# Kernel optimization log

Measured on AMD Instinct MI355X. Metric: run time of the kernel, lower is better.

The kernel has to match this reference:

```python
import jax, jax.numpy as jnp
import numpy as np

E, CAP, D = 32, 4096, 256
H = 4 * D  # hidden_dim = 4*d_model


def setup_inputs() -> dict:
    key = jax.random.key(0)
    k1, k2, k3 = jax.random.split(key, 3)
    x = jax.random.normal(k1, (E, CAP, D), dtype=jnp.float32)
    w_fc = jax.random.normal(k2, (E, D, H), dtype=jnp.float32) * (1.0 / np.sqrt(D))
    w_proj = jax.random.normal(k3, (E, H, D), dtype=jnp.float32) * (1.0 / np.sqrt(H))
    return {"x": x, "w_fc": w_fc, "w_proj": w_proj}


def reference(x, w_fc, w_proj):
    # h = bmm(x, w_fc): [E, cap, d] @ [E, d, 4d] -> [E, cap, 4d]
    h = jnp.einsum('ecd,edh->ech', x, w_fc)
    # exact GELU (torch nn.GELU default uses erf form)
    h = jax.nn.gelu(h, approximate=False)
    # out = bmm(h, w_proj): [E, cap, 4d] @ [E, 4d, d] -> [E, cap, d]
    out = jnp.einsum('ech,ehd->ecd', h, w_proj)
    # dropout is identity in eval mode (p=0.0 here)
    return out
```

## Files before the change

kernel.cpp:

```cpp
#include <hip/hip_runtime.h>
#include <cstdint>
#include <cstddef>


#define NE   32
#define CAPN 4096
#define DDIM 256
#define HDIM 1024

typedef __bf16 bf16x8 __attribute__((ext_vector_type(8)));
typedef __bf16 bf16x4 __attribute__((ext_vector_type(4)));
typedef __bf16 bf16x2 __attribute__((ext_vector_type(2)));
typedef float  f32x4  __attribute__((ext_vector_type(4)));

#define XS_OFF   0
#define STG_OFF  65536
#define STG_SZ   16384
#define HC_OFF   98304
#define LDS_BYTES 131072

#define AS1 __attribute__((address_space(1)))
#define AS3 __attribute__((address_space(3)))

__device__ __forceinline__ void gld_lds16(const void* g, void* l) {
  __builtin_amdgcn_global_load_lds((const AS1 uint32_t*)g, (AS3 uint32_t*)l, 16, 0, 0);
}

__device__ __forceinline__ float gelu_f(float x) {
  float x2 = x * x;
  float u  = x * __builtin_fmaf(0.1029432f, x2, 2.3022078f);
  float t  = __builtin_amdgcn_exp2f(u);
  float r  = __builtin_amdgcn_rcpf(t + 1.0f);
  return __builtin_fmaf(-x, r, x);
}

__global__ __launch_bounds__(256) void tcast_kernel(const float* __restrict__ in,
                                                    __bf16* __restrict__ outp,
                                                    int R, int C) {
  __shared__ __bf16 tl[64][72];
  const int cb = C >> 6;
  const int nb = (R >> 6) * cb;
  const int b  = blockIdx.x;
  const int e  = b / nb;
  const int t  = b - e * nb;
  const int br = t / cb;
  const int bc = t - br * cb;
  const float* src = in + ((size_t)e * R + (size_t)br * 64) * C + (size_t)bc * 64;
#pragma unroll
  for (int i = 0; i < 16; ++i) {
    int idx = i * 256 + threadIdx.x;
    int r = idx >> 6, c = idx & 63;
    tl[c][r] = (__bf16)src[(size_t)r * C + c];
  }
  __syncthreads();
  __bf16* dst = outp + ((size_t)e * C + (size_t)bc * 64) * R + (size_t)br * 64;
#pragma unroll
  for (int i = 0; i < 8; ++i) {
    int idx = i * 512 + threadIdx.x * 2;
    int c = idx >> 6, r = idx & 63;
    bf16x2 p;
    p[0] = tl[c][r];
    p[1] = tl[c][r + 1];
    *(bf16x2*)(dst + (size_t)c * R + r) = p;
  }
}

__global__ __launch_bounds__(512, 2) void fused_mlp(
    const float* __restrict__ x, const __bf16* __restrict__ wfcT,
    const __bf16* __restrict__ wprojT, float* __restrict__ out) {
  extern __shared__ char smem[];
  const int tid  = threadIdx.x;
  const int lane = tid & 63;
  const int l15  = lane & 15;
  const int l4   = lane >> 4;
  const int w    = tid >> 6;
  const int wm   = w & 1;
  const int q    = w >> 1;
  const int bid  = blockIdx.x;
  const int e    = bid >> 5;
  const int m0   = (bid & 31) << 7;

  auto stage_slab = [&](int s) {
    const int buf = s & 1;
    const int c   = s >> 3;
    const int t   = s & 7;
    const __bf16* base;
    size_t rs;
    if (t < 4) {
      base = wfcT + (size_t)(e * HDIM + c * 128) * DDIM + t * 64;
      rs   = DDIM;
    } else {
      const int j = t - 4;
      base = wprojT + (size_t)(e * DDIM + (j & 1) * 128) * HDIM + c * 128 + (j >> 1) * 64;
      rs   = HDIM;
    }
#pragma unroll
    for (int i = 0; i < 2; ++i) {
      int o  = tid + i * 512;
      int r  = o >> 3;
      int sl = (o & 7) ^ (r & 7);
      gld_lds16(base + (size_t)r * rs + sl * 8, &smem[STG_OFF + buf * STG_SZ + o * 16]);
    }
  };

  {
    const float* xb = x + ((size_t)(e * CAPN + m0)) * DDIM;
#pragma unroll
    for (int i = 0; i < 8; ++i) {
      int f2  = i * 512 + tid;
      int row = f2 >> 5;
      int s   = f2 & 31;
      const float4 a0 = *(const float4*)(xb + (size_t)row * DDIM + s * 8);
      const float4 a1 = *(const float4*)(xb + (size_t)row * DDIM + s * 8 + 4);
      bf16x8 v;
      v[0] = (__bf16)a0.x; v[1] = (__bf16)a0.y; v[2] = (__bf16)a0.z; v[3] = (__bf16)a0.w;
      v[4] = (__bf16)a1.x; v[5] = (__bf16)a1.y; v[6] = (__bf16)a1.z; v[7] = (__bf16)a1.w;
      int phys = (s & 24) | ((s & 7) ^ (row & 7));
      *(bf16x8*)(&smem[XS_OFF + row * 512 + phys * 16]) = v;
    }
  }

  stage_slab(0);
  stage_slab(1);

  f32x4 zero = 0.0f;
  f32x4 acc2[4][4];
#pragma unroll
  for (int a = 0; a < 4; ++a)
#pragma unroll
    for (int b = 0; b < 4; ++b) acc2[a][b] = zero;

#define SLAB_PRE(lastp)                                                        \
  do {                                                                         \
    if (lastp) asm volatile("s_waitcnt vmcnt(0) lgkmcnt(0)" ::: "memory");     \
    else       asm volatile("s_waitcnt vmcnt(2) lgkmcnt(0)" ::: "memory");     \
    __builtin_amdgcn_s_barrier();                                              \
    __builtin_amdgcn_sched_barrier(0);                                         \
  } while (0)

#define SLAB_POST(sidx)                                                        \
  do {                                                                         \
    __builtin_amdgcn_sched_barrier(0);                                         \
    __builtin_amdgcn_s_barrier();                                              \
    if ((sidx) + 2 < 64) stage_slab((sidx) + 2);                               \
  } while (0)

  for (int c = 0; c < 8; ++c) {
    f32x4 acc1[2][4];
#pragma unroll
    for (int a = 0; a < 2; ++a)
#pragma unroll
      for (int b = 0; b < 4; ++b) acc1[a][b] = zero;

#pragma unroll
    for (int ks = 0; ks < 4; ++ks) {
      const int sidx = c * 8 + ks;
      const int buf  = sidx & 1;
      SLAB_PRE(false);
      bf16x8 a0[2], a1[2], b0[4], b1[4];
#pragma unroll
      for (int fh = 0; fh < 2; ++fh) {
        int r = q * 32 + fh * 16 + l15;
        a0[fh] = *(const bf16x8*)(&smem[STG_OFF + buf * STG_SZ + r * 128 + ((0 * 4 + l4) ^ (r & 7)) * 16]);
        a1[fh] = *(const bf16x8*)(&smem[STG_OFF + buf * STG_SZ + r * 128 + ((1 * 4 + l4) ^ (r & 7)) * 16]);
      }
#pragma unroll
      for (int fm = 0; fm < 4; ++fm) {
        int m   = wm * 64 + fm * 16 + l15;
        int sl0 = ks * 8 + 0 * 4 + l4;
        int sl1 = ks * 8 + 1 * 4 + l4;
        int p0  = (sl0 & 24) | ((sl0 & 7) ^ (m & 7));
        int p1  = (sl1 & 24) | ((sl1 & 7) ^ (m & 7));
        b0[fm] = *(const bf16x8*)(&smem[XS_OFF + m * 512 + p0 * 16]);
        b1[fm] = *(const bf16x8*)(&smem[XS_OFF + m * 512 + p1 * 16]);
      }
      __builtin_amdgcn_s_setprio(1);
#pragma unroll
      for (int fh = 0; fh < 2; ++fh)
#pragma unroll
        for (int fm = 0; fm < 4; ++fm)
          acc1[fh][fm] = __builtin_amdgcn_mfma_f32_16x16x32_bf16(a0[fh], b0[fm], acc1[fh][fm], 0, 0, 0);
#pragma unroll
      for (int fh = 0; fh < 2; ++fh)
#pragma unroll
        for (int fm = 0; fm < 4; ++fm)
          acc1[fh][fm] = __builtin_amdgcn_mfma_f32_16x16x32_bf16(a1[fh], b1[fm], acc1[fh][fm], 0, 0, 0);
      __builtin_amdgcn_s_setprio(0);
      SLAB_POST(sidx);
    }

#pragma unroll
    for (int fh = 0; fh < 2; ++fh) {
#pragma unroll
      for (int fm = 0; fm < 4; ++fm) {
        int m  = wm * 64 + fm * 16 + l15;
        int hl = q * 32 + fh * 16 + l4 * 4;
        bf16x4 hv;
#pragma unroll
        for (int j = 0; j < 4; ++j) hv[j] = (__bf16)gelu_f(acc1[fh][fm][j]);
        int sl   = hl >> 3;
        int half = (hl >> 2) & 1;
        int ph   = (sl & 8) | ((sl & 7) ^ (m & 7));
        *(bf16x4*)(&smem[HC_OFF + m * 256 + ph * 16 + half * 8]) = hv;
      }
    }

#pragma unroll
    for (int j = 0; j < 4; ++j) {
      const int sidx = c * 8 + 4 + j;
      const int buf  = sidx & 1;
      const int hd   = j & 1;
      const int hh   = j >> 1;
      const bool last = (c == 7) && (j == 3);
      SLAB_PRE(last);
      bf16x8 a0[2], a1[2], b0[4], b1[4];
#pragma unroll
      for (int fd = 0; fd < 2; ++fd) {
        int r = q * 32 + fd * 16 + l15;
        a0[fd] = *(const bf16x8*)(&smem[STG_OFF + buf * STG_SZ + r * 128 + ((0 * 4 + l4) ^ (r & 7)) * 16]);
        a1[fd] = *(const bf16x8*)(&smem[STG_OFF + buf * STG_SZ + r * 128 + ((1 * 4 + l4) ^ (r & 7)) * 16]);
      }
#pragma unroll
      for (int fm = 0; fm < 4; ++fm) {
        int m   = wm * 64 + fm * 16 + l15;
        int sl0 = hh * 8 + 0 * 4 + l4;
        int sl1 = hh * 8 + 1 * 4 + l4;
        int p0  = (sl0 & 8) | ((sl0 & 7) ^ (m & 7));
        int p1  = (sl1 & 8) | ((sl1 & 7) ^ (m & 7));
        b0[fm] = *(const bf16x8*)(&smem[HC_OFF + m * 256 + p0 * 16]);
        b1[fm] = *(const bf16x8*)(&smem[HC_OFF + m * 256 + p1 * 16]);
      }
      __builtin_amdgcn_s_setprio(1);
#pragma unroll
      for (int fd = 0; fd < 2; ++fd)
#pragma unroll
        for (int fm = 0; fm < 4; ++fm)
          acc2[hd * 2 + fd][fm] = __builtin_amdgcn_mfma_f32_16x16x32_bf16(a0[fd], b0[fm], acc2[hd * 2 + fd][fm], 0, 0, 0);
#pragma unroll
      for (int fd = 0; fd < 2; ++fd)
#pragma unroll
        for (int fm = 0; fm < 4; ++fm)
          acc2[hd * 2 + fd][fm] = __builtin_amdgcn_mfma_f32_16x16x32_bf16(a1[fd], b1[fm], acc2[hd * 2 + fd][fm], 0, 0, 0);
      __builtin_amdgcn_s_setprio(0);
      SLAB_POST(sidx);
    }
  }

#pragma unroll
  for (int a = 0; a < 4; ++a) {
#pragma unroll
    for (int fm = 0; fm < 4; ++fm) {
      int m = m0 + wm * 64 + fm * 16 + l15;
      int d = (a >> 1) * 128 + q * 32 + (a & 1) * 16 + l4 * 4;
      *(f32x4*)(out + ((size_t)(e * CAPN + m)) * DDIM + d) = acc2[a][fm];
    }
  }
}

extern "C" void kernel_launch(void* const* d_in, const int* in_sizes, int n_in,
                              void* d_out, int out_size, void* d_ws, size_t ws_size,
                              hipStream_t stream) {
  (void)in_sizes; (void)n_in; (void)out_size; (void)ws_size;
  const float* x     = (const float*)d_in[0];
  const float* wfc   = (const float*)d_in[1];
  const float* wproj = (const float*)d_in[2];
  float* out = (float*)d_out;

  __bf16* wfcT   = (__bf16*)d_ws;
  __bf16* wprojT = (__bf16*)((char*)d_ws + (size_t)NE * DDIM * HDIM * sizeof(__bf16));

  hipFuncSetAttribute((const void*)fused_mlp,
                      hipFuncAttributeMaxDynamicSharedMemorySize, LDS_BYTES);

  tcast_kernel<<<dim3(NE * 64), dim3(256), 0, stream>>>(wfc, wfcT, DDIM, HDIM);
  tcast_kernel<<<dim3(NE * 64), dim3(256), 0, stream>>>(wproj, wprojT, HDIM, DDIM);
  fused_mlp<<<dim3(NE * 32), dim3(512), LDS_BYTES, stream>>>(x, wfcT, wprojT, out);
}
```

Before: 243.9 us.

## Add 160KB-LDS fused MLP variant with 256-wide hidden chunks

Adds a new fused MLP kernel that uses 160KB of LDS to hold a full 128x256 hidden chunk and processes the hidden dimension in 4 chunks of 256 instead of 8 of 128. It uses a 4x4 MFMA tile per wave with thinner 32-wide k slabs. Larger hidden chunks reduce the number of GELU/phase transitions and let each wave cover more output per slab. The cost is occupancy, which drops from 2 blocks to 1 block per CU, leaving less latency hiding. The old 128KB kernel stays as a fallback if the larger LDS attribute is rejected.

```diff
diff --git a/kernel.cpp b/kernel.cpp
--- a/kernel.cpp
+++ b/kernel.cpp
@@ -12,12 +12,6 @@
 typedef __bf16 bf16x4 __attribute__((ext_vector_type(4)));
 typedef __bf16 bf16x2 __attribute__((ext_vector_type(2)));
 typedef float  f32x4  __attribute__((ext_vector_type(4)));
-
-#define XS_OFF   0
-#define STG_OFF  65536
-#define STG_SZ   16384
-#define HC_OFF   98304
-#define LDS_BYTES 131072
 
 #define AS1 __attribute__((address_space(1)))
 #define AS3 __attribute__((address_space(3)))
@@ -33,6 +27,28 @@
   float r  = __builtin_amdgcn_rcpf(t + 1.0f);
   return __builtin_fmaf(-x, r, x);
 }
+
+#define SLAB_PRE(lastp)                                                        \
+  do {                                                                         \
+    if (lastp) asm volatile("s_waitcnt vmcnt(0) lgkmcnt(0)" ::: "memory");     \
+    else       asm volatile("s_waitcnt vmcnt(2) lgkmcnt(0)" ::: "memory");     \
+    __builtin_amdgcn_s_barrier();                                              \
+    __builtin_amdgcn_sched_barrier(0);                                         \
+  } while (0)
+
+#define SLAB_POST_160(sidx)                                                    \
+  do {                                                                         \
+    __builtin_amdgcn_sched_barrier(0);                                         \
+    __builtin_amdgcn_s_barrier();                                              \
+    if ((sidx) + 2 < 64) stage_slab((sidx) + 2);                               \
+  } while (0)
+
+#define SLAB_POST_128(sidx)                                                    \
+  do {                                                                         \
+    __builtin_amdgcn_sched_barrier(0);                                         \
+    __builtin_amdgcn_s_barrier();                                              \
+    if ((sidx) + 2 < 64) stage_slab((sidx) + 2);                               \
+  } while (0)
 
 __global__ __launch_bounds__(256) void tcast_kernel(const float* __restrict__ in,
                                                     __bf16* __restrict__ outp,
@@ -65,7 +81,13 @@
   }
 }
 
-__global__ __launch_bounds__(512, 2) void fused_mlp(
+#define B_XS   0
+#define B_HC   65536
+#define B_STG  131072
+#define STG_SZ 16384
+#define LDS160 163840
+
+__global__ __launch_bounds__(512, 1) void fused_mlp_160(
     const float* __restrict__ x, const __bf16* __restrict__ wfcT,
     const __bf16* __restrict__ wprojT, float* __restrict__ out) {
   extern __shared__ char smem[];
@@ -80,6 +102,168 @@
   const int e    = bid >> 5;
   const int m0   = (bid & 31) << 7;
 
+  const int physA = l4 ^ ((l15 >> 1) & 3);
+  const int aBase = B_STG + q * 4096 + l15 * 64 + physA * 16;
+  const int mRow  = wm * 64 + l15;
+  const int m7    = l15 & 7;
+
+  auto stage_slab = [&](int s) {
+    const int buf = s & 1;
+    const int c   = s >> 4;
+    const int t   = s & 15;
+    const __bf16* base;
+    size_t rs;
+    if (t < 8) {
+      base = wfcT + (size_t)(e * HDIM + c * 256) * DDIM + t * 32;
+      rs   = DDIM;
+    } else {
+      base = wprojT + (size_t)(e * DDIM) * HDIM + c * 256 + (t - 8) * 32;
+      rs   = HDIM;
+    }
+#pragma unroll
+    for (int i = 0; i < 2; ++i) {
+      int o  = tid + i * 512;
+      int r  = o >> 2;
+      int sl = (o & 3) ^ ((r >> 1) & 3);
+      gld_lds16(base + (size_t)r * rs + sl * 8, &smem[B_STG + buf * STG_SZ + o * 16]);
+    }
+  };
+
+  {
+    const float* xb = x + ((size_t)(e * CAPN + m0)) * DDIM;
+#pragma unroll
+    for (int i = 0; i < 8; ++i) {
+      int f2  = i * 512 + tid;
+      int row = f2 >> 5;
+      int s   = f2 & 31;
+      const float4 a0 = *(const float4*)(xb + (size_t)row * DDIM + s * 8);
+      const float4 a1 = *(const float4*)(xb + (size_t)row * DDIM + s * 8 + 4);
+      bf16x8 v;
+      v[0] = (__bf16)a0.x; v[1] = (__bf16)a0.y; v[2] = (__bf16)a0.z; v[3] = (__bf16)a0.w;
+      v[4] = (__bf16)a1.x; v[5] = (__bf16)a1.y; v[6] = (__bf16)a1.z; v[7] = (__bf16)a1.w;
+      int phys = (s & 24) | ((s & 7) ^ (row & 7));
+      *(bf16x8*)(&smem[B_XS + row * 512 + phys * 16]) = v;
+    }
+  }
+
+  stage_slab(0);
+  stage_slab(1);
+
+  f32x4 zero = 0.0f;
+  f32x4 acc2[4][4];
+#pragma unroll
+  for (int a = 0; a < 4; ++a)
+#pragma unroll
+    for (int b = 0; b < 4; ++b) acc2[a][b] = zero;
+
+  for (int c = 0; c < 4; ++c) {
+    f32x4 acc1[4][4];
+#pragma unroll
+    for (int a = 0; a < 4; ++a)
+#pragma unroll
+      for (int b = 0; b < 4; ++b) acc1[a][b] = zero;
+
+#pragma unroll
+    for (int ds = 0; ds < 8; ++ds) {
+      const int sidx = c * 16 + ds;
+      const int buf  = ds & 1;
+      SLAB_PRE(false);
+      bf16x8 af[4], bx[4];
+#pragma unroll
+      for (int f = 0; f < 4; ++f)
+        af[f] = *(const bf16x8*)(&smem[aBase + buf * STG_SZ + f * 1024]);
+#pragma unroll
+      for (int fm = 0; fm < 4; ++fm) {
+        int s  = ds * 4 + l4;
+        int ph = (s & 24) | ((s & 7) ^ m7);
+        bx[fm] = *(const bf16x8*)(&smem[B_XS + (mRow + fm * 16) * 512 + ph * 16]);
+      }
+      __builtin_amdgcn_s_setprio(1);
+#pragma unroll
+      for (int fa = 0; fa < 4; ++fa)
+#pragma unroll
+        for (int fm = 0; fm < 4; ++fm)
+          acc1[fa][fm] = __builtin_amdgcn_mfma_f32_16x16x32_bf16(
+              af[fa], bx[fm], acc1[fa][fm], 0, 0, 0);
+      __builtin_amdgcn_s_setprio(0);
+      SLAB_POST_160(sidx);
+    }
+
+#pragma unroll
+    for (int fa = 0; fa < 4; ++fa) {
+#pragma unroll
+      for (int fm = 0; fm < 4; ++fm) {
+        int m  = mRow + fm * 16;
+        int s  = q * 8 + fa * 2 + (l4 >> 1);
+        int hf = l4 & 1;
+        bf16x4 hv;
+#pragma unroll
+        for (int j = 0; j < 4; ++j) hv[j] = (__bf16)gelu_f(acc1[fa][fm][j]);
+        int ph = (s & 24) | ((s & 7) ^ (m & 7));
+        *(bf16x4*)(&smem[B_HC + m * 512 + ph * 16 + hf * 8]) = hv;
+      }
+    }
+
+#pragma unroll
+    for (int hs = 0; hs < 8; ++hs) {
+      const int sidx = c * 16 + 8 + hs;
+      const int buf  = hs & 1;
+      const bool last = (hs == 7) && (c == 3);
+      SLAB_PRE(last);
+      bf16x8 af[4], bx[4];
+#pragma unroll
+      for (int f = 0; f < 4; ++f)
+        af[f] = *(const bf16x8*)(&smem[aBase + buf * STG_SZ + f * 1024]);
+#pragma unroll
+      for (int fm = 0; fm < 4; ++fm) {
+        int s  = hs * 4 + l4;
+        int ph = (s & 24) | ((s & 7) ^ m7);
+        bx[fm] = *(const bf16x8*)(&smem[B_HC + (mRow + fm * 16) * 512 + ph * 16]);
+      }
+      __builtin_amdgcn_s_setprio(1);
+#pragma unroll
+      for (int fd = 0; fd < 4; ++fd)
+#pragma unroll
+        for (int fm = 0; fm < 4; ++fm)
+          acc2[fd][fm] = __builtin_amdgcn_mfma_f32_16x16x32_bf16(
+              af[fd], bx[fm], acc2[fd][fm], 0, 0, 0);
+      __builtin_amdgcn_s_setprio(0);
+      SLAB_POST_160(sidx);
+    }
+  }
+
+#pragma unroll
+  for (int fd = 0; fd < 4; ++fd) {
+#pragma unroll
+    for (int fm = 0; fm < 4; ++fm) {
+      int m = m0 + mRow + fm * 16;
+      int d = q * 64 + fd * 16 + l4 * 4;
+      *(f32x4*)(out + ((size_t)(e * CAPN + m)) * DDIM + d) = acc2[fd][fm];
+    }
+  }
+}
+
+#define F_XS   0
+#define F_STG  65536
+#define F_SSZ  16384
+#define F_HC   98304
+#define LDS128 131072
+
+__global__ __launch_bounds__(512, 2) void fused_mlp_128(
+    const float* __restrict__ x, const __bf16* __restrict__ wfcT,
+    const __bf16* __restrict__ wprojT, float* __restrict__ out) {
+  extern __shared__ char smem[];
+  const int tid  = threadIdx.x;
+  const int lane = tid & 63;
+  const int l15  = lane & 15;
+  const int l4   = lane >> 4;
+  const int w    = tid >> 6;
+  const int wm   = w & 1;
+  const int q    = w >> 1;
+  const int bid  = blockIdx.x;
+  const int e    = bid >> 5;
+  const int m0   = (bid & 31) << 7;
+
   auto stage_slab = [&](int s) {
     const int buf = s & 1;
     const int c   = s >> 3;
@@ -99,7 +283,7 @@
       int o  = tid + i * 512;
       int r  = o >> 3;
       int sl = (o & 7) ^ (r & 7);
-      gld_lds16(base + (size_t)r * rs + sl * 8, &smem[STG_OFF + buf * STG_SZ + o * 16]);
+      gld_lds16(base + (size_t)r * rs + sl * 8, &smem[F_STG + buf * F_SSZ + o * 16]);
     }
   };
 
@@ -116,7 +300,7 @@
       v[0] = (__bf16)a0.x; v[1] = (__bf16)a0.y; v[2] = (__bf16)a0.z; v[3] = (__bf16)a0.w;
       v[4] = (__bf16)a1.x; v[5] = (__bf16)a1.y; v[6] = (__bf16)a1.z; v[7] = (__bf16)a1.w;
       int phys = (s & 24) | ((s & 7) ^ (row & 7));
-      *(bf16x8*)(&smem[XS_OFF + row * 512 + phys * 16]) = v;
+      *(bf16x8*)(&smem[F_XS + row * 512 + phys * 16]) = v;
     }
   }
 
@@ -129,21 +313,6 @@
   for (int a = 0; a < 4; ++a)
 #pragma unroll
     for (int b = 0; b < 4; ++b) acc2[a][b] = zero;
-
-#define SLAB_PRE(lastp)                                                        \
-  do {                                                                         \
-    if (lastp) asm volatile("s_waitcnt vmcnt(0) lgkmcnt(0)" ::: "memory");     \
-    else       asm volatile("s_waitcnt vmcnt(2) lgkmcnt(0)" ::: "memory");     \
-    __builtin_amdgcn_s_barrier();                                              \
-    __builtin_amdgcn_sched_barrier(0);                                         \
-  } while (0)
-
-#define SLAB_POST(sidx)                                                        \
-  do {                                                                         \
-    __builtin_amdgcn_sched_barrier(0);                                         \
-    __builtin_amdgcn_s_barrier();                                              \
-    if ((sidx) + 2 < 64) stage_slab((sidx) + 2);                               \
-  } while (0)
 
   for (int c = 0; c < 8; ++c) {
     f32x4 acc1[2][4];
@@ -161,8 +330,8 @@
 #pragma unroll
       for (int fh = 0; fh < 2; ++fh) {
         int r = q * 32 + fh * 16 + l15;
-        a0[fh] = *(const bf16x8*)(&smem[STG_OFF + buf * STG_SZ + r * 128 + ((0 * 4 + l4) ^ (r & 7)) * 16]);
-        a1[fh] = *(const bf16x8*)(&smem[STG_OFF + buf * STG_SZ + r * 128 + ((1 * 4 + l4) ^ (r & 7)) * 16]);
+        a0[fh] = *(const bf16x8*)(&smem[F_STG + buf * F_SSZ + r * 128 + ((0 * 4 + l4) ^ (r & 7)) * 16]);
+        a1[fh] = *(const bf16x8*)(&smem[F_STG + buf * F_SSZ + r * 128 + ((1 * 4 + l4) ^ (r & 7)) * 16]);
       }
 #pragma unroll
       for (int fm = 0; fm < 4; ++fm) {
@@ -171,8 +340,8 @@
         int sl1 = ks * 8 + 1 * 4 + l4;
         int p0  = (sl0 & 24) | ((sl0 & 7) ^ (m & 7));
         int p1  = (sl1 & 24) | ((sl1 & 7) ^ (m & 7));
-        b0[fm] = *(const bf16x8*)(&smem[XS_OFF + m * 512 + p0 * 16]);
-        b1[fm] = *(const bf16x8*)(&smem[XS_OFF + m * 512 + p1 * 16]);
+        b0[fm] = *(const bf16x8*)(&smem[F_XS + m * 512 + p0 * 16]);
+        b1[fm] = *(const bf16x8*)(&smem[F_XS + m * 512 + p1 * 16]);
       }
       __builtin_amdgcn_s_setprio(1);
 #pragma unroll
@@ -186,7 +355,7 @@
         for (int fm = 0; fm < 4; ++fm)
           acc1[fh][fm] = __builtin_amdgcn_mfma_f32_16x16x32_bf16(a1[fh], b1[fm], acc1[fh][fm], 0, 0, 0);
       __builtin_amdgcn_s_setprio(0);
-      SLAB_POST(sidx);
+      SLAB_POST_128(sidx);
     }
 
 #pragma unroll
@@ -201,7 +370,7 @@
         int sl   = hl >> 3;
         int half = (hl >> 2) & 1;
         int ph   = (sl & 8) | ((sl & 7) ^ (m & 7));
-        *(bf16x4*)(&smem[HC_OFF + m * 256 + ph * 16 + half * 8]) = hv;
+        *(bf16x4*)(&smem[F_HC + m * 256 + ph * 16 + half * 8]) = hv;
       }
     }
 
@@ -217,8 +386,8 @@
 #pragma unroll
       for (int fd = 0; fd < 2; ++fd) {
         int r = q * 32 + fd * 16 + l15;
-        a0[fd] = *(const bf16x8*)(&smem[STG_OFF + buf * STG_SZ + r * 128 + ((0 * 4 + l4) ^ (r & 7)) * 16]);
-        a1[fd] = *(const bf16x8*)(&smem[STG_OFF + buf * STG_SZ + r * 128 + ((1 * 4 + l4) ^ (r & 7)) * 16]);
+        a0[fd] = *(const bf16x8*)(&smem[F_STG + buf * F_SSZ + r * 128 + ((0 * 4 + l4) ^ (r & 7)) * 16]);
+        a1[fd] = *(const bf16x8*)(&smem[F_STG + buf * F_SSZ + r * 128 + ((1 * 4 + l4) ^ (r & 7)) * 16]);
       }
 #pragma unroll
       for (int fm = 0; fm < 4; ++fm) {
@@ -227,8 +396,8 @@
         int sl1 = hh * 8 + 1 * 4 + l4;
         int p0  = (sl0 & 8) | ((sl0 & 7) ^ (m & 7));
         int p1  = (sl1 & 8) | ((sl1 & 7) ^ (m & 7));
-        b0[fm] = *(const bf16x8*)(&smem[HC_OFF + m * 256 + p0 * 16]);
-        b1[fm] = *(const bf16x8*)(&smem[HC_OFF + m * 256 + p1 * 16]);
+        b0[fm] = *(const bf16x8*)(&smem[F_HC + m * 256 + p0 * 16]);
+        b1[fm] = *(const bf16x8*)(&smem[F_HC + m * 256 + p1 * 16]);
       }
       __builtin_amdgcn_s_setprio(1);
 #pragma unroll
@@ -242,7 +411,7 @@
         for (int fm = 0; fm < 4; ++fm)
           acc2[hd * 2 + fd][fm] = __builtin_amdgcn_mfma_f32_16x16x32_bf16(a1[fd], b1[fm], acc2[hd * 2 + fd][fm], 0, 0, 0);
       __builtin_amdgcn_s_setprio(0);
-      SLAB_POST(sidx);
+      SLAB_POST_128(sidx);
     }
   }
 
@@ -269,10 +438,16 @@
   __bf16* wfcT   = (__bf16*)d_ws;
   __bf16* wprojT = (__bf16*)((char*)d_ws + (size_t)NE * DDIM * HDIM * sizeof(__bf16));
 
-  hipFuncSetAttribute((const void*)fused_mlp,
-                      hipFuncAttributeMaxDynamicSharedMemorySize, LDS_BYTES);
-
   tcast_kernel<<<dim3(NE * 64), dim3(256), 0, stream>>>(wfc, wfcT, DDIM, HDIM);
   tcast_kernel<<<dim3(NE * 64), dim3(256), 0, stream>>>(wproj, wprojT, HDIM, DDIM);
-  fused_mlp<<<dim3(NE * 32), dim3(512), LDS_BYTES, stream>>>(x, wfcT, wprojT, out);
-}
+
+  hipError_t e160 = hipFuncSetAttribute(
+      (const void*)fused_mlp_160, hipFuncAttributeMaxDynamicSharedMemorySize, LDS160);
+  if (e160 == hipSuccess) {
+    fused_mlp_160<<<dim3(NE * 32), dim3(512), LDS160, stream>>>(x, wfcT, wprojT, out);
+  } else {
+    hipFuncSetAttribute((const void*)fused_mlp_128,
+                        hipFuncAttributeMaxDynamicSharedMemorySize, LDS128);
+    fused_mlp_128<<<dim3(NE * 32), dim3(512), LDS128, stream>>>(x, wfcT, wprojT, out);
+  }
+}
```

After: 228.1 us. -6.5%, faster.
